# Kernel tuning notes

Hardware: AMD Instinct MI355X
Metric: run time of the kernel (lower is better)

## Reference

```python
import jax, jax.numpy as jnp
import numpy as np

N, C_TOTAL, C, H, W = 8, 448, 100, 56, 56


def setup_inputs() -> dict:
    key = jax.random.key(0)
    k1, k2, k3, k4 = jax.random.split(key, 4)
    fmaps = jax.random.normal(k1, (N, C_TOTAL, H, W), dtype=jnp.float32)
    select_index = jax.random.randint(k2, (C,), 0, C_TOTAL)
    mean = jax.random.normal(k3, (C, H, W), dtype=jnp.float32)
    # Per-pixel inverse covariance must be PSD so the quadratic form is >= 0
    A = jax.random.normal(k4, (C, C, H, W), dtype=jnp.float32)
    cov = jnp.einsum('cehw,dehw->cdhw', A, A) / jnp.float32(C)  # (C,C,H,W), PSD per pixel
    return {
        'fmaps': fmaps,
        'select_index': select_index,
        'mean': mean,
        'cov': cov,
        'min_score': jnp.float32(0.0),
        'max_score': jnp.float32(50.0),
    }


def reference(fmaps, select_index, mean, cov, min_score, max_score):
    # x_ = fmaps[:, select_index, ...] - mean  -> (N, C, H, W)
    x = fmaps[:, select_index, :, :] - mean[None]
    # left = sum_c x[n,c,h,w] * cov[c,d,h,w]  (per-pixel matvec), avoids (N,C,C,H,W) intermediate
    left = jnp.einsum('nchw,cdhw->ndhw', x, cov)
    # per-pixel Mahalanobis distance
    s_map = jnp.sqrt(jnp.sum(x * left, axis=1))  # (N, H, W)
    # bilinear upsample x4 (torch Upsample align_corners=False == half-pixel linear resize)
    score_map = jax.image.resize(s_map, (s_map.shape[0], 4 * H, 4 * W), method='linear')
    scores = (score_map - min_score) / (max_score - min_score)
    return jnp.squeeze(scores)
```

## Files before the change

### kernel.cpp

```cpp
#include <hip/hip_runtime.h>
#include <math.h>

#define NN 8
#define C_TOTAL 448
#define CC 100
#define HH 56
#define WW 56
#define HW (HH*WW)
#define NPIX4 (HW/4)
#define OH 224
#define OW 224
#define NPAIR 50
#define NT4 13

__device__ __forceinline__ void fma4(float4& acc, const float4 a, const float4 b) {
    acc.x = fmaf(a.x, b.x, acc.x);
    acc.y = fmaf(a.y, b.y, acc.y);
    acc.z = fmaf(a.z, b.z, acc.z);
    acc.w = fmaf(a.w, b.w, acc.w);
}

__global__ __launch_bounds__(256) void prep_x_kernel(
    const float* __restrict__ fmaps, const int* __restrict__ sel,
    const float* __restrict__ mean, float* __restrict__ xbuf)
{
    const int idx = blockIdx.x * 256 + threadIdx.x;
    const int total = NN * CC * NPIX4;
    if (idx >= total) return;
    const int p4 = idx % NPIX4;
    const int c  = (idx / NPIX4) % CC;
    const int n  = idx / (NPIX4 * CC);

    const float4* f4 = (const float4*)fmaps;
    const float4* m4 = (const float4*)mean;
    float4*       x4 = (float4*)xbuf;

    const float4 f = f4[((size_t)n * C_TOTAL + sel[c]) * NPIX4 + p4];
    const float4 m = m4[(size_t)c * NPIX4 + p4];
    float4 r;
    r.x = f.x - m.x; r.y = f.y - m.y; r.z = f.z - m.z; r.w = f.w - m.w;
    x4[((size_t)n * CC + c) * NPIX4 + p4] = r;
}

__global__ __launch_bounds__(512) void qform_kernel(
    const float* __restrict__ xbuf, const float* __restrict__ cov,
    float* __restrict__ qpart)
{
    const int tile = blockIdx.x % NT4;
    const int r    = blockIdx.x / NT4;
    const int s    = 99 - r;
    const int n    = threadIdx.x >> 6;
    const int p4   = tile * 64 + (threadIdx.x & 63);
    if (p4 >= NPIX4) return;

    const float4* x4  = (const float4*)xbuf + (size_t)n * CC * NPIX4;
    const float4* c4  = (const float4*)cov;

    const float4* covr = c4 + ((size_t)r * CC + r) * NPIX4 + p4;
    const float4* covs = c4 + ((size_t)s * CC + s) * NPIX4 + p4;
    const float4* xp   = x4 + (size_t)r * NPIX4 + p4;

    float4 ir = make_float4(0.f, 0.f, 0.f, 0.f);
    float4 is = make_float4(0.f, 0.f, 0.f, 0.f);

    float4 xr = *xp;
    {
        float4 h; h.x = 0.5f*xr.x; h.y = 0.5f*xr.y; h.z = 0.5f*xr.z; h.w = 0.5f*xr.w;
        fma4(ir, h, *covr);
    }
    xp += NPIX4; covr += NPIX4;

#pragma unroll 4
    for (int d = r + 1; d < s; ++d) {
        const float4 xd = *xp;
        fma4(ir, xd, *covr);
        xp += NPIX4; covr += NPIX4;
    }

    float4 xs = *xp;
    fma4(ir, xs, *covr);
    {
        float4 h; h.x = 0.5f*xs.x; h.y = 0.5f*xs.y; h.z = 0.5f*xs.z; h.w = 0.5f*xs.w;
        fma4(is, h, *covs);
    }
    xp += NPIX4; covr += NPIX4; covs += NPIX4;

#pragma unroll 4
    for (int d = s + 1; d < CC; ++d) {
        const float4 xd = *xp;
        fma4(ir, xd, *covr);
        fma4(is, xd, *covs);
        xp += NPIX4; covr += NPIX4; covs += NPIX4;
    }

    float4 q;
    q.x = 2.0f * (fmaf(xr.x, ir.x, xs.x * is.x));
    q.y = 2.0f * (fmaf(xr.y, ir.y, xs.y * is.y));
    q.z = 2.0f * (fmaf(xr.z, ir.z, xs.z * is.z));
    q.w = 2.0f * (fmaf(xr.w, ir.w, xs.w * is.w));

    float4* qp = (float4*)qpart;
    qp[((size_t)r * NN + n) * NPIX4 + p4] = q;
}

__global__ __launch_bounds__(256) void reduce_kernel(
    const float* __restrict__ qpart, float* __restrict__ smap)
{
    const int idx = blockIdx.x * 256 + threadIdx.x;
    if (idx >= NN * NPIX4) return;
    const int p4 = idx % NPIX4;
    const int n  = idx / NPIX4;

    const float4* qp = (const float4*)qpart;
    float4 acc = make_float4(0.f, 0.f, 0.f, 0.f);
#pragma unroll
    for (int k = 0; k < NPAIR; ++k) {
        const float4 v = qp[((size_t)k * NN + n) * NPIX4 + p4];
        acc.x += v.x; acc.y += v.y; acc.z += v.z; acc.w += v.w;
    }
    float4 o;
    o.x = sqrtf(fmaxf(acc.x, 0.f));
    o.y = sqrtf(fmaxf(acc.y, 0.f));
    o.z = sqrtf(fmaxf(acc.z, 0.f));
    o.w = sqrtf(fmaxf(acc.w, 0.f));
    ((float4*)smap)[(size_t)n * NPIX4 + p4] = o;
}

__global__ __launch_bounds__(256) void upsample_kernel(
    const float* __restrict__ smap,
    const float* __restrict__ minp, const float* __restrict__ maxp,
    float* __restrict__ out)
{
    const int idx = blockIdx.x * 256 + threadIdx.x;
    const int total = NN * OH * OW;
    if (idx >= total) return;

    const int ox = idx % OW;
    const int oy = (idx / OW) % OH;
    const int n  = idx / (OW * OH);

    const float fy = oy * 0.25f - 0.375f;
    const float fx = ox * 0.25f - 0.375f;

    int y0 = (int)floorf(fy);
    int x0 = (int)floorf(fx);
    const float wy = fy - (float)y0;
    const float wx = fx - (float)x0;
    int y1 = min(y0 + 1, HH - 1); y0 = max(y0, 0);
    int x1 = min(x0 + 1, WW - 1); x0 = max(x0, 0);

    const float* s = smap + (size_t)n * HW;
    const float v00 = s[y0 * WW + x0];
    const float v01 = s[y0 * WW + x1];
    const float v10 = s[y1 * WW + x0];
    const float v11 = s[y1 * WW + x1];

    const float v = (1.0f - wy) * ((1.0f - wx) * v00 + wx * v01)
                  +          wy * ((1.0f - wx) * v10 + wx * v11);

    const float mn = *minp;
    const float mx = *maxp;
    out[idx] = (v - mn) / (mx - mn);
}

extern "C" void kernel_launch(void* const* d_in, const int* in_sizes, int n_in,
                              void* d_out, int out_size, void* d_ws, size_t ws_size,
                              hipStream_t stream)
{
    const float* fmaps = (const float*)d_in[0];
    const int*   sel   = (const int*)  d_in[1];
    const float* mean  = (const float*)d_in[2];
    const float* cov   = (const float*)d_in[3];
    const float* minp  = (const float*)d_in[4];
    const float* maxp  = (const float*)d_in[5];
    float* out = (float*)d_out;

    float* xbuf  = (float*)d_ws;
    float* qpart = xbuf + (size_t)NN * CC * HW;
    float* smap  = qpart + (size_t)NPAIR * NN * HW;

    {
        const int total = NN * CC * NPIX4;
        prep_x_kernel<<<(total + 255) / 256, 256, 0, stream>>>(fmaps, sel, mean, xbuf);
    }
    qform_kernel<<<NT4 * NPAIR, 512, 0, stream>>>(xbuf, cov, qpart);
    {
        const int total = NN * NPIX4;
        reduce_kernel<<<(total + 255) / 256, 256, 0, stream>>>(qpart, smap);
    }
    {
        const int total = NN * OH * OW;
        upsample_kernel<<<(total + 255) / 256, 256, 0, stream>>>(smap, minp, maxp, out);
    }
}
```

Baseline: 247.5 us.

## Reuse covariance across batch per thread, store centered features as fp16

The quadratic-form kernel now has each thread accumulate all 8 batch images for its pixel quad. Each covariance load is reused eight times in registers instead of being fetched once per batch warp. The inner d loop is split across the 8 warps, and the partial sums are combined through an LDS reduction. The centered features are stored as fp16, interleaved by batch, which halves their bandwidth but loses precision in the Mahalanobis sum.

```diff
diff --git a/kernel.cpp b/kernel.cpp
--- a/kernel.cpp
+++ b/kernel.cpp
@@ -13,94 +13,114 @@
 #define NPAIR 50
 #define NT4 13
 
+typedef __attribute__((ext_vector_type(4))) _Float16 half4;
+
 __device__ __forceinline__ void fma4(float4& acc, const float4 a, const float4 b) {
     acc.x = fmaf(a.x, b.x, acc.x);
     acc.y = fmaf(a.y, b.y, acc.y);
     acc.z = fmaf(a.z, b.z, acc.z);
     acc.w = fmaf(a.w, b.w, acc.w);
 }
+__device__ __forceinline__ float4 h2f(const half4 h) {
+    float4 r; r.x = (float)h.x; r.y = (float)h.y; r.z = (float)h.z; r.w = (float)h.w;
+    return r;
+}
 
 __global__ __launch_bounds__(256) void prep_x_kernel(
     const float* __restrict__ fmaps, const int* __restrict__ sel,
-    const float* __restrict__ mean, float* __restrict__ xbuf)
+    const float* __restrict__ mean, half4* __restrict__ xbuf)
 {
     const int idx = blockIdx.x * 256 + threadIdx.x;
-    const int total = NN * CC * NPIX4;
-    if (idx >= total) return;
-    const int p4 = idx % NPIX4;
-    const int c  = (idx / NPIX4) % CC;
-    const int n  = idx / (NPIX4 * CC);
+    if (idx >= CC * NPIX4) return;
+    const int quad = idx % NPIX4;
+    const int c    = idx / NPIX4;
 
     const float4* f4 = (const float4*)fmaps;
-    const float4* m4 = (const float4*)mean;
-    float4*       x4 = (float4*)xbuf;
-
-    const float4 f = f4[((size_t)n * C_TOTAL + sel[c]) * NPIX4 + p4];
-    const float4 m = m4[(size_t)c * NPIX4 + p4];
-    float4 r;
-    r.x = f.x - m.x; r.y = f.y - m.y; r.z = f.z - m.z; r.w = f.w - m.w;
-    x4[((size_t)n * CC + c) * NPIX4 + p4] = r;
-}
-
-__global__ __launch_bounds__(512) void qform_kernel(
-    const float* __restrict__ xbuf, const float* __restrict__ cov,
+    const float4  m  = ((const float4*)mean)[(size_t)c * NPIX4 + quad];
+    const int     sc = sel[c];
+
+    half4 hv[NN];
+#pragma unroll
+    for (int n = 0; n < NN; ++n) {
+        const float4 f = f4[((size_t)n * C_TOTAL + sc) * NPIX4 + quad];
+        half4 h;
+        h.x = (_Float16)(f.x - m.x);
+        h.y = (_Float16)(f.y - m.y);
+        h.z = (_Float16)(f.z - m.z);
+        h.w = (_Float16)(f.w - m.w);
+        hv[n] = h;
+    }
+    half4* dst = xbuf + ((size_t)c * NPIX4 + quad) * NN;
+#pragma unroll
+    for (int n = 0; n < NN; ++n) dst[n] = hv[n];
+}
+
+__global__ __launch_bounds__(512, 4) void qform_kernel(
+    const half4* __restrict__ xbuf, const float* __restrict__ cov,
     float* __restrict__ qpart)
 {
+    __shared__ float4 lred[NN * NN * 64];
+
     const int tile = blockIdx.x % NT4;
     const int r    = blockIdx.x / NT4;
-    const int s    = 99 - r;
-    const int n    = threadIdx.x >> 6;
-    const int p4   = tile * 64 + (threadIdx.x & 63);
-    if (p4 >= NPIX4) return;
-
-    const float4* x4  = (const float4*)xbuf + (size_t)n * CC * NPIX4;
-    const float4* c4  = (const float4*)cov;
-
-    const float4* covr = c4 + ((size_t)r * CC + r) * NPIX4 + p4;
-    const float4* covs = c4 + ((size_t)s * CC + s) * NPIX4 + p4;
-    const float4* xp   = x4 + (size_t)r * NPIX4 + p4;
-
-    float4 ir = make_float4(0.f, 0.f, 0.f, 0.f);
-    float4 is = make_float4(0.f, 0.f, 0.f, 0.f);
-
-    float4 xr = *xp;
-    {
-        float4 h; h.x = 0.5f*xr.x; h.y = 0.5f*xr.y; h.z = 0.5f*xr.z; h.w = 0.5f*xr.w;
-        fma4(ir, h, *covr);
-    }
-    xp += NPIX4; covr += NPIX4;
-
-#pragma unroll 4
-    for (int d = r + 1; d < s; ++d) {
-        const float4 xd = *xp;
-        fma4(ir, xd, *covr);
-        xp += NPIX4; covr += NPIX4;
-    }
-
-    float4 xs = *xp;
-    fma4(ir, xs, *covr);
-    {
-        float4 h; h.x = 0.5f*xs.x; h.y = 0.5f*xs.y; h.z = 0.5f*xs.z; h.w = 0.5f*xs.w;
-        fma4(is, h, *covs);
-    }
-    xp += NPIX4; covr += NPIX4; covs += NPIX4;
-
-#pragma unroll 4
-    for (int d = s + 1; d < CC; ++d) {
-        const float4 xd = *xp;
-        fma4(ir, xd, *covr);
-        fma4(is, xd, *covs);
-        xp += NPIX4; covr += NPIX4; covs += NPIX4;
-    }
-
-    float4 q;
-    q.x = 2.0f * (fmaf(xr.x, ir.x, xs.x * is.x));
-    q.y = 2.0f * (fmaf(xr.y, ir.y, xs.y * is.y));
-    q.z = 2.0f * (fmaf(xr.z, ir.z, xs.z * is.z));
-    q.w = 2.0f * (fmaf(xr.w, ir.w, xs.w * is.w));
-
-    float4* qp = (float4*)qpart;
-    qp[((size_t)r * NN + n) * NPIX4 + p4] = q;
+    const int s    = CC - 1 - r;
+    const int w    = threadIdx.x >> 6;
+    const int lane = threadIdx.x & 63;
+    const int qraw = tile * 64 + lane;
+    const bool valid = qraw < NPIX4;
+    const int quad = valid ? qraw : (NPIX4 - 1);
+
+    const float4* c4 = (const float4*)cov;
+
+    float4 part[NN];
+#pragma unroll
+    for (int n = 0; n < NN; ++n) part[n] = make_float4(0.f, 0.f, 0.f, 0.f);
+
+    for (int seg = 0; seg < 2; ++seg) {
+        const int row = seg ? s : r;
+
+        float4 acc[NN];
+#pragma unroll
+        for (int n = 0; n < NN; ++n) acc[n] = make_float4(0.f, 0.f, 0.f, 0.f);
+
+        for (int d = row + w; d < CC; d += NN) {
+            float4 cv = c4[((size_t)row * CC + d) * NPIX4 + quad];
+            if (d == row) { cv.x *= 0.5f; cv.y *= 0.5f; cv.z *= 0.5f; cv.w *= 0.5f; }
+            const half4* xp = xbuf + ((size_t)d * NPIX4 + quad) * NN;
+            half4 hv[NN];
+#pragma unroll
+            for (int n = 0; n < NN; ++n) hv[n] = xp[n];
+#pragma unroll
+            for (int n = 0; n < NN; ++n) fma4(acc[n], h2f(hv[n]), cv);
+        }
+
+        const half4* xrp = xbuf + ((size_t)row * NPIX4 + quad) * NN;
+#pragma unroll
+        for (int n = 0; n < NN; ++n) {
+            const float4 xr = h2f(xrp[n]);
+            part[n].x = fmaf(2.f * xr.x, acc[n].x, part[n].x);
+            part[n].y = fmaf(2.f * xr.y, acc[n].y, part[n].y);
+            part[n].z = fmaf(2.f * xr.z, acc[n].z, part[n].z);
+            part[n].w = fmaf(2.f * xr.w, acc[n].w, part[n].w);
+        }
+    }
+
+#pragma unroll
+    for (int n = 0; n < NN; ++n) lred[(w * NN + n) * 64 + lane] = part[n];
+    __syncthreads();
+
+    {
+        const int n = w;
+        float4 sum = make_float4(0.f, 0.f, 0.f, 0.f);
+#pragma unroll
+        for (int ww = 0; ww < NN; ++ww) {
+            const float4 v = lred[(ww * NN + n) * 64 + lane];
+            sum.x += v.x; sum.y += v.y; sum.z += v.z; sum.w += v.w;
+        }
+        if (valid) {
+            ((float4*)qpart)[((size_t)r * NN + n) * NPIX4 + qraw] = sum;
+        }
+    }
 }
 
 __global__ __launch_bounds__(256) void reduce_kernel(
@@ -175,12 +195,12 @@
     const float* maxp  = (const float*)d_in[5];
     float* out = (float*)d_out;
 
-    float* xbuf  = (float*)d_ws;
-    float* qpart = xbuf + (size_t)NN * CC * HW;
+    half4* xbuf  = (half4*)d_ws;
+    float* qpart = (float*)((char*)d_ws + (size_t)CC*NPIX4*NN*8);
     float* smap  = qpart + (size_t)NPAIR * NN * HW;
 
     {
-        const int total = NN * CC * NPIX4;
+        const int total = CC * NPIX4;
         prep_x_kernel<<<(total + 255) / 256, 256, 0, stream>>>(fmaps, sel, mean, xbuf);
     }
     qform_kernel<<<NT4 * NPAIR, 512, 0, stream>>>(xbuf, cov, qpart);
```

New measurement: 228.2 us. -7.8%, faster.
